# Optimization experiments

Hardware: AMD Instinct MI355X
Metric: run time of the kernel (lower is better)

## Reference

```python
import jax, jax.numpy as jnp
import numpy as np

B, S, D = 4, 2048, 1024
H, K = 16, 64
EPS = 1e-3  # Keras LayerNormalization default epsilon


def setup_inputs() -> dict:
    key = jax.random.key(0)
    ks = jax.random.split(key, 11)
    s = 0.02
    return {
        "x":  jax.random.normal(ks[0], (B, S, D), jnp.float32),
        "Wq": jax.random.normal(ks[1], (D, H, K), jnp.float32) * s,
        "bq": jnp.zeros((H, K), jnp.float32),
        "Wk": jax.random.normal(ks[2], (D, H, K), jnp.float32) * s,
        "bk": jnp.zeros((H, K), jnp.float32),
        "Wv": jax.random.normal(ks[3], (D, H, K), jnp.float32) * s,
        "bv": jnp.zeros((H, K), jnp.float32),
        "Wo": jax.random.normal(ks[4], (H, K, D), jnp.float32) * s,
        "bo": jnp.zeros((D,), jnp.float32),
        "gamma": jnp.ones((D,), jnp.float32),
        "beta":  jnp.zeros((D,), jnp.float32),
    }


def reference(x, Wq, bq, Wk, bk, Wv, bv, Wo, bo, gamma, beta):
    # QKV projections (Keras MHA einsum form): [B,S,D] -> [B,S,H,K]
    q = jnp.einsum("bsd,dhk->bshk", x, Wq) + bq
    k = jnp.einsum("bsd,dhk->bshk", x, Wk) + bk
    v = jnp.einsum("bsd,dhk->bshk", x, Wv) + bv
    scale = 1.0 / jnp.sqrt(jnp.asarray(K, x.dtype))
    scores = jnp.einsum("bqhk,bshk->bhqs", q, k) * scale  # [B,H,S,S]
    attn = jax.nn.softmax(scores, axis=-1)
    ctx = jnp.einsum("bhqs,bshk->bqhk", attn, v)           # [B,S,H,K]
    attn_out = jnp.einsum("bqhk,hkd->bqd", ctx, Wo) + bo   # [B,S,D]
    # residual + LayerNorm (over last axis)
    y = x + attn_out
    mu = jnp.mean(y, axis=-1, keepdims=True)
    var = jnp.mean(jnp.square(y - mu), axis=-1, keepdims=True)
    return (y - mu) * jax.lax.rsqrt(var + EPS) * gamma + beta
```

## Files before the change

### kernel.cpp

```cpp
#include <hip/hip_runtime.h>

typedef float f32x4 __attribute__((ext_vector_type(4)));
typedef float f32x16 __attribute__((ext_vector_type(16)));
typedef __bf16 bf16x8 __attribute__((ext_vector_type(8)));
typedef __bf16 bf16x4 __attribute__((ext_vector_type(4)));
typedef __bf16 bf16x2 __attribute__((ext_vector_type(2)));
typedef unsigned short us4 __attribute__((ext_vector_type(4)));

#define DEV __device__ __forceinline__

DEV unsigned short f2bf(float f) {
  union { float f; unsigned int u; } v; v.f = f;
  unsigned int u = v.u;
  return (unsigned short)((u + 0x7FFFu + ((u >> 16) & 1u)) >> 16);
}

typedef const __attribute__((address_space(1))) void* gvp;
typedef __attribute__((address_space(3))) void* lvp;

DEV void gll16(const void* g, void* l) {
  __builtin_amdgcn_global_load_lds((gvp)g, (lvp)l, 16, 0, 0);
}

DEV float fexp2(float x) { return __builtin_amdgcn_exp2f(x); }

DEV void plswap(unsigned& a, unsigned& b) {
  asm("v_permlane32_swap_b32 %0, %1" : "+v"(a), "+v"(b));
}
DEV float xhalf_sum(float v) {
  union { float f; unsigned u; } a, b;
  a.f = v; b.f = v;
  plswap(a.u, b.u);
  return a.f + b.f;
}

__global__ void k_convert(const float* __restrict__ in, unsigned short* __restrict__ out, int n4) {
  int i = blockIdx.x * blockDim.x + threadIdx.x;
  if (i < n4) {
    float4 v = ((const float4*)in)[i];
    us4 o = { f2bf(v.x), f2bf(v.y), f2bf(v.z), f2bf(v.w) };
    ((us4*)out)[i] = o;
  }
}

__global__ void k_transpose4(const float* __restrict__ w0, const float* __restrict__ w1,
                             const float* __restrict__ w2, const float* __restrict__ w3,
                             unsigned short* __restrict__ o0, unsigned short* __restrict__ o1,
                             unsigned short* __restrict__ o2, unsigned short* __restrict__ o3) {
  const float* in = (blockIdx.z == 0) ? w0 : (blockIdx.z == 1) ? w1 : (blockIdx.z == 2) ? w2 : w3;
  unsigned short* out = (blockIdx.z == 0) ? o0 : (blockIdx.z == 1) ? o1 : (blockIdx.z == 2) ? o2 : o3;
  __shared__ float tile[32][33];
  const int bx = blockIdx.x * 32, by = blockIdx.y * 32;
  const int tx = threadIdx.x, ty = threadIdx.y;
#pragma unroll
  for (int r = 0; r < 4; ++r)
    tile[ty + r * 8][tx] = in[(size_t)(by + ty + r * 8) * 1024 + bx + tx];
  __syncthreads();
#pragma unroll
  for (int r = 0; r < 4; ++r)
    out[(size_t)(bx + ty + r * 8) * 1024 + by + tx] = f2bf(tile[tx][ty + r * 8]);
}

__global__ void k_gemm_qkv(const unsigned short* __restrict__ xb,
                           const unsigned short* __restrict__ wqt,
                           const unsigned short* __restrict__ wkt,
                           const unsigned short* __restrict__ wvt,
                           const float* __restrict__ bq, const float* __restrict__ bk,
                           const float* __restrict__ bv,
                           unsigned short* __restrict__ qb, unsigned short* __restrict__ kb,
                           unsigned short* __restrict__ vtb) {
  __shared__ unsigned short As[128 * 64];
  __shared__ unsigned short Bs[128 * 64];
  const int tid = threadIdx.x;
  const int lane = tid & 63;
  const int wave = tid >> 6;
  const int l15 = lane & 15;
  const int lq  = lane >> 4;
  const int wm = wave >> 1, wn = wave & 1;
  const int z = blockIdx.z;

  const unsigned short* A;
  const unsigned short* Bt;
  int mbase, nbase;
  if (z == 2) { A = wvt; Bt = xb; mbase = blockIdx.y * 128; nbase = blockIdx.x * 128; }
  else        { A = xb; Bt = z ? wkt : wqt; mbase = blockIdx.x * 128; nbase = blockIdx.y * 128; }

  f32x4 acc[4][4] = {};

  for (int kt = 0; kt < 1024; kt += 64) {
    __syncthreads();
#pragma unroll
    for (int c = 0; c < 4; ++c) {
      int e = (c * 256 + tid) * 8;
      int row = e >> 6;
      int o2 = (e * 2) ^ ((row & 7) << 4);
      int col = (o2 >> 1) & 63;
      gll16(A + (size_t)(mbase + row) * 1024 + kt + col,
            As + (c * 256 + (tid & ~63)) * 8);
      gll16(Bt + (size_t)(nbase + row) * 1024 + kt + col,
            Bs + (c * 256 + (tid & ~63)) * 8);
    }
    __syncthreads();
#pragma unroll
    for (int ks = 0; ks < 2; ++ks) {
      bf16x8 af[4], bfv[4];
#pragma unroll
      for (int i = 0; i < 4; ++i) {
        int row = wm * 64 + i * 16 + l15;
        int off = row * 128 + ((((ks << 2) | lq) ^ (row & 7)) << 4);
        af[i] = *(const bf16x8*)((const char*)As + off);
      }
#pragma unroll
      for (int j = 0; j < 4; ++j) {
        int row = wn * 64 + j * 16 + l15;
        int off = row * 128 + ((((ks << 2) | lq) ^ (row & 7)) << 4);
        bfv[j] = *(const bf16x8*)((const char*)Bs + off);
      }
#pragma unroll
      for (int i = 0; i < 4; ++i)
#pragma unroll
        for (int j = 0; j < 4; ++j)
          acc[i][j] = __builtin_amdgcn_mfma_f32_16x16x32_bf16(af[i], bfv[j], acc[i][j], 0, 0, 0);
    }
  }

  const float scale = (z == 0) ? 0.18033688011112042f : 1.0f;
  const float* bias = (z == 0) ? bq : (z == 1) ? bk : bv;
  unsigned short* outp = (z == 0) ? qb : (z == 1) ? kb : vtb;

#pragma unroll
  for (int i = 0; i < 4; ++i) {
#pragma unroll
    for (int j = 0; j < 4; ++j) {
#pragma unroll
      for (int r = 0; r < 4; ++r) {
        int mi = mbase + wm * 64 + i * 16 + lq * 4 + r;
        int nj = nbase + wn * 64 + j * 16 + l15;
        float v = acc[i][j][r];
        if (z < 2) {
          v = (v + bias[nj]) * scale;
          int b = mi >> 11, s = mi & 2047, h = nj >> 6, kk = nj & 63;
          outp[(((size_t)((b << 4) + h) * 2048 + s) << 6) + kk] = f2bf(v);
        } else {
          v = v + bias[mi];
          int h = mi >> 6, d = mi & 63, b = nj >> 11, s = nj & 2047;
          outp[(((size_t)((b << 4) + h) << 6) + d) * 2048 + s] = f2bf(v);
        }
      }
    }
  }
}

__global__ void k_gemm_out(const unsigned short* __restrict__ A,
                           const unsigned short* __restrict__ Bt,
                           const float* __restrict__ bias,
                           float* __restrict__ outp,
                           const float* __restrict__ xres) {
  __shared__ unsigned short As[128 * 64];
  __shared__ unsigned short Bs[128 * 64];
  const int tid = threadIdx.x;
  const int lane = tid & 63;
  const int wave = tid >> 6;
  const int l15 = lane & 15;
  const int lq  = lane >> 4;
  const int wm = wave >> 1, wn = wave & 1;
  const int mbase = blockIdx.x * 128;
  const int nbase = blockIdx.y * 128;

  f32x4 acc[4][4] = {};

  for (int kt = 0; kt < 1024; kt += 64) {
    __syncthreads();
#pragma unroll
    for (int c = 0; c < 4; ++c) {
      int e = (c * 256 + tid) * 8;
      int row = e >> 6;
      int o2 = (e * 2) ^ ((row & 7) << 4);
      int col = (o2 >> 1) & 63;
      gll16(A + (size_t)(mbase + row) * 1024 + kt + col,
            As + (c * 256 + (tid & ~63)) * 8);
      gll16(Bt + (size_t)(nbase + row) * 1024 + kt + col,
            Bs + (c * 256 + (tid & ~63)) * 8);
    }
    __syncthreads();
#pragma unroll
    for (int ks = 0; ks < 2; ++ks) {
      bf16x8 af[4], bfv[4];
#pragma unroll
      for (int i = 0; i < 4; ++i) {
        int row = wm * 64 + i * 16 + l15;
        int off = row * 128 + ((((ks << 2) | lq) ^ (row & 7)) << 4);
        af[i] = *(const bf16x8*)((const char*)As + off);
      }
#pragma unroll
      for (int j = 0; j < 4; ++j) {
        int row = wn * 64 + j * 16 + l15;
        int off = row * 128 + ((((ks << 2) | lq) ^ (row & 7)) << 4);
        bfv[j] = *(const bf16x8*)((const char*)Bs + off);
      }
#pragma unroll
      for (int i = 0; i < 4; ++i)
#pragma unroll
        for (int j = 0; j < 4; ++j)
          acc[i][j] = __builtin_amdgcn_mfma_f32_16x16x32_bf16(af[i], bfv[j], acc[i][j], 0, 0, 0);
    }
  }

#pragma unroll
  for (int i = 0; i < 4; ++i)
#pragma unroll
    for (int j = 0; j < 4; ++j)
#pragma unroll
      for (int r = 0; r < 4; ++r) {
        int mi = mbase + wm * 64 + i * 16 + lq * 4 + r;
        int nj = nbase + wn * 64 + j * 16 + l15;
        size_t idx = (size_t)mi * 1024 + nj;
        outp[idx] = acc[i][j][r] + bias[nj] + xres[idx];
      }
}

__global__ __launch_bounds__(256, 4) void k_attn(const unsigned short* __restrict__ q,
                       const unsigned short* __restrict__ k,
                       const unsigned short* __restrict__ vt,
                       unsigned short* __restrict__ ctx) {
  __shared__ unsigned short KV[2][2][64 * 64];

  const int tid = threadIdx.x;
  const int lane = tid & 63;
  const int wave = tid >> 6;
  const int l31 = lane & 31;
  const int l5 = lane >> 5;

  const int bid = blockIdx.x;
  const int swz = (bid & 7) * 128 + (bid >> 3);
  const int bh = swz >> 4;
  const int qtile = swz & 15;
  const int qbase = qtile * 128;
  const size_t sl = (size_t)bh << 17;

  const int qrow = qbase + wave * 32 + l31;
  bf16x8 qreg[4];
#pragma unroll
  for (int ds = 0; ds < 4; ++ds)
    qreg[ds] = *(const bf16x8*)(q + sl + (size_t)qrow * 64 + ds * 16 + l5 * 8);

#define STAGE_KV(BUF, TT) do {                                                 \
    const int kvb_ = (TT) * 64;                                                \
    _Pragma("unroll")                                                          \
    for (int c = 0; c < 2; ++c) {                                              \
      int e = (c * 256 + tid) * 8;                                             \
      int row_ = e >> 6;                                                       \
      int o2 = (e * 2) ^ ((row_ & 7) << 4);                                    \
      int col_ = (o2 >> 1) & 63;                                               \
      gll16(k + sl + (size_t)(kvb_ + row_) * 64 + col_,                        \
            KV[BUF][0] + (c * 256 + (tid & ~63)) * 8);                         \
      gll16(vt + sl + (size_t)row_ * 2048 + kvb_ + col_,                       \
            KV[BUF][1] + (c * 256 + (tid & ~63)) * 8);                         \
    }                                                                          \
  } while (0)

  STAGE_KV(0, 0);
  __syncthreads();

  f32x16 acc0 = {}, acc1 = {};
  float lrow = 0.f;

  for (int t = 0; t < 32; ++t) {
    const int cur = t & 1;
    if (t < 31) STAGE_KV(cur ^ 1, t + 1);

    const char* Ksc = (const char*)KV[cur][0];
    const char* Vtc = (const char*)KV[cur][1];

    bf16x8 kf0[4], kf1[4];
#pragma unroll
    for (int ds = 0; ds < 4; ++ds) {
      int r0 = l31, r1 = 32 + l31;
      kf0[ds] = *(const bf16x8*)(Ksc + r0 * 128 + ((ds * 32 + l5 * 16) ^ ((r0 & 7) << 4)));
      kf1[ds] = *(const bf16x8*)(Ksc + r1 * 128 + ((ds * 32 + l5 * 16) ^ ((r1 & 7) << 4)));
    }
    f32x16 s0 = {}, s1 = {};
    __builtin_amdgcn_s_setprio(1);
#pragma unroll
    for (int ds = 0; ds < 4; ++ds)
      s0 = __builtin_amdgcn_mfma_f32_32x32x16_bf16(kf0[ds], qreg[ds], s0, 0, 0, 0);
#pragma unroll
    for (int ds = 0; ds < 4; ++ds)
      s1 = __builtin_amdgcn_mfma_f32_32x32x16_bf16(kf1[ds], qreg[ds], s1, 0, 0, 0);
    __builtin_amdgcn_s_setprio(0);
    __builtin_amdgcn_sched_barrier(0);

    unsigned pk0[8], pk1[8];
    float r0s = 0.f, r1s = 0.f, r2s = 0.f, r3s = 0.f;
#pragma unroll
    for (int m = 0; m < 8; ++m) {
      float a0 = fexp2(s0[2 * m]), a1 = fexp2(s0[2 * m + 1]);
      float b0 = fexp2(s1[2 * m]), b1 = fexp2(s1[2 * m + 1]);
      r0s += a0; r1s += a1; r2s += b0; r3s += b1;
      union { bf16x2 v; unsigned u; } ua, ub;
      ua.v = bf16x2{ (__bf16)a0, (__bf16)a1 };
      ub.v = bf16x2{ (__bf16)b0, (__bf16)b1 };
      pk0[m] = ua.u; pk1[m] = ub.u;
    }
    lrow += (r0s + r1s) + (r2s + r3s);
    __builtin_amdgcn_sched_barrier(0);

    bf16x8 av0[4], av1[4];
#pragma unroll
    for (int kvg = 0; kvg < 4; ++kvg) {
      int r0 = l31, r1 = 32 + l31;
      av0[kvg] = *(const bf16x8*)(Vtc + r0 * 128 + ((kvg * 32 + l5 * 16) ^ ((r0 & 7) << 4)));
      av1[kvg] = *(const bf16x8*)(Vtc + r1 * 128 + ((kvg * 32 + l5 * 16) ^ ((r1 & 7) << 4)));
    }
#pragma unroll
    for (int kvh = 0; kvh < 2; ++kvh) {
      unsigned* pk = kvh ? pk1 : pk0;
#pragma unroll
      for (int g = 0; g < 2; ++g) {
        unsigned a0_ = pk[4 * g],     b0_ = pk[4 * g + 2];
        unsigned a1_ = pk[4 * g + 1], b1_ = pk[4 * g + 3];
        plswap(a0_, b0_);
        plswap(a1_, b1_);
        union { unsigned u[4]; bf16x8 v; } pf;
        pf.u[0] = a0_; pf.u[1] = a1_; pf.u[2] = b0_; pf.u[3] = b1_;
        const int kvg = 2 * kvh + g;
        __builtin_amdgcn_s_setprio(1);
        acc0 = __builtin_amdgcn_mfma_f32_32x32x16_bf16(av0[kvg], pf.v, acc0, 0, 0, 0);
        acc1 = __builtin_amdgcn_mfma_f32_32x32x16_bf16(av1[kvg], pf.v, acc1, 0, 0, 0);
        __builtin_amdgcn_s_setprio(0);
      }
    }

    __syncthreads();
  }

  const float inv = 1.f / xhalf_sum(lrow);

  unsigned short* TR = (unsigned short*)KV;
  const int qloc = wave * 32 + l31;
  const int swq = (qloc & 7) << 4;
#pragma unroll
  for (int dh = 0; dh < 2; ++dh) {
    const f32x16& ac = dh ? acc1 : acc0;
#pragma unroll
    for (int g3 = 0; g3 < 4; ++g3) {
      bf16x4 o4 = { (__bf16)(ac[4 * g3] * inv), (__bf16)(ac[4 * g3 + 1] * inv),
                    (__bf16)(ac[4 * g3 + 2] * inv), (__bf16)(ac[4 * g3 + 3] * inv) };
      *(bf16x4*)((char*)TR + qloc * 128 + ((dh * 64 + g3 * 16 + l5 * 8) ^ swq)) = o4;
    }
  }
  __syncthreads();

  const int b = bh >> 4, h = bh & 15;
  {
    int row = tid >> 1, half = tid & 1;
    int sw = (row & 7) << 4;
    unsigned short* gdst = ctx + (size_t)(b * 2048 + qbase + row) * 1024 + h * 64 + half * 32;
#pragma unroll
    for (int i = 0; i < 4; ++i) {
      bf16x8 vv = *(const bf16x8*)((const char*)TR + row * 128 + ((half * 64 + i * 16) ^ sw));
      *(bf16x8*)(gdst + i * 8) = vv;
    }
  }
#undef STAGE_KV
}

__global__ void k_ln(const float* __restrict__ y, const float* __restrict__ gamma,
                     const float* __restrict__ beta, float* __restrict__ out) {
  const int row = blockIdx.x;
  const int tid = threadIdx.x;
  const float4 v = ((const float4*)(y + (size_t)row * 1024))[tid];
  float sum = v.x + v.y + v.z + v.w;
  float sq = v.x * v.x + v.y * v.y + v.z * v.z + v.w * v.w;
#pragma unroll
  for (int m = 1; m <= 32; m <<= 1) {
    sum += __shfl_xor(sum, m);
    sq  += __shfl_xor(sq, m);
  }
  __shared__ float s1[4], s2[4];
  const int wv = tid >> 6, lane = tid & 63;
  if (lane == 0) { s1[wv] = sum; s2[wv] = sq; }
  __syncthreads();
  sum = s1[0] + s1[1] + s1[2] + s1[3];
  sq  = s2[0] + s2[1] + s2[2] + s2[3];
  const float mu = sum * (1.f / 1024.f);
  const float rs = rsqrtf(sq * (1.f / 1024.f) - mu * mu + 1e-3f);
  const float4 g  = ((const float4*)gamma)[tid];
  const float4 bb = ((const float4*)beta)[tid];
  float4 o;
  o.x = (v.x - mu) * rs * g.x + bb.x;
  o.y = (v.y - mu) * rs * g.y + bb.y;
  o.z = (v.z - mu) * rs * g.z + bb.z;
  o.w = (v.w - mu) * rs * g.w + bb.w;
  ((float4*)(out + (size_t)row * 1024))[tid] = o;
}

extern "C" void kernel_launch(void* const* d_in, const int* in_sizes, int n_in,
                              void* d_out, int out_size, void* d_ws, size_t ws_size,
                              hipStream_t stream) {
  const float* x  = (const float*)d_in[0];
  const float* Wq = (const float*)d_in[1];
  const float* bq = (const float*)d_in[2];
  const float* Wk = (const float*)d_in[3];
  const float* bk = (const float*)d_in[4];
  const float* Wv = (const float*)d_in[5];
  const float* bv = (const float*)d_in[6];
  const float* Wo = (const float*)d_in[7];
  const float* bo = (const float*)d_in[8];
  const float* gamma = (const float*)d_in[9];
  const float* beta  = (const float*)d_in[10];
  float* out = (float*)d_out;

  char* ws = (char*)d_ws;
  const size_t MB = 1024 * 1024;
  unsigned short* xb  = (unsigned short*)(ws);
  unsigned short* wqt = (unsigned short*)(ws + 16 * MB);
  unsigned short* wkt = (unsigned short*)(ws + 18 * MB);
  unsigned short* wvt = (unsigned short*)(ws + 20 * MB);
  unsigned short* wot = (unsigned short*)(ws + 22 * MB);
  unsigned short* qb  = (unsigned short*)(ws + 24 * MB);
  unsigned short* kb  = (unsigned short*)(ws + 40 * MB);
  unsigned short* vtb = (unsigned short*)(ws + 56 * MB);
  unsigned short* ctx = (unsigned short*)(ws + 72 * MB);
  float* yb = (float*)(ws + 24 * MB);

  k_convert<<<8192, 256, 0, stream>>>(x, xb, 2097152);
  dim3 tb(32, 8), tg(32, 32, 4);
  k_transpose4<<<tg, tb, 0, stream>>>(Wq, Wk, Wv, Wo, wqt, wkt, wvt, wot);

  k_gemm_qkv<<<dim3(64, 8, 3), 256, 0, stream>>>(xb, wqt, wkt, wvt, bq, bk, bv, qb, kb, vtb);

  k_attn<<<1024, 256, 0, stream>>>(qb, kb, vtb, ctx);

  k_gemm_out<<<dim3(64, 8), 256, 0, stream>>>(ctx, wot, bo, yb, x);

  k_ln<<<8192, 256, 0, stream>>>(yb, gamma, beta, out);
  (void)in_sizes; (void)n_in; (void)out_size; (void)ws_size;
}
```

Measured before the change: 196.6 us.

## Fuse Q and K projections into a double-buffered 256x256 tile GEMM

After: 206.2 us. 4.9% more time.

```diff
diff --git a/kernel.cpp b/kernel.cpp
--- a/kernel.cpp
+++ b/kernel.cpp
@@ -61,14 +61,127 @@
     out[(size_t)(bx + ty + r * 8) * 1024 + by + tx] = f2bf(tile[tx][ty + r * 8]);
 }
 
-__global__ void k_gemm_qkv(const unsigned short* __restrict__ xb,
-                           const unsigned short* __restrict__ wqt,
-                           const unsigned short* __restrict__ wkt,
-                           const unsigned short* __restrict__ wvt,
-                           const float* __restrict__ bq, const float* __restrict__ bk,
-                           const float* __restrict__ bv,
-                           unsigned short* __restrict__ qb, unsigned short* __restrict__ kb,
-                           unsigned short* __restrict__ vtb) {
+__global__ __launch_bounds__(512, 1) void k_gemm8_qk(
+    const unsigned short* __restrict__ A,
+    const unsigned short* __restrict__ Bt,
+    const float* __restrict__ bq, const float* __restrict__ bk,
+    unsigned short* __restrict__ qb, unsigned short* __restrict__ kb) {
+  __shared__ unsigned short LA[2][256 * 64];
+  __shared__ unsigned short LB[2][256 * 64];
+  const int tid = threadIdx.x;
+  const int lane = tid & 63;
+  const int wave = tid >> 6;
+  const int l15 = lane & 15;
+  const int lq = lane >> 4;
+  const int wm = wave >> 2;
+  const int wn = wave & 3;
+
+  const int lin = blockIdx.x + (blockIdx.y << 5);
+  const int swz = (lin & 7) * 32 + (lin >> 3);
+  const int mt = swz & 31, nt = swz >> 5;
+  const int mbase = mt * 256, nbase = nt * 256;
+
+  f32x4 acc[8][4] = {};
+
+#define STAGE8(BUF, TT) do {                                                   \
+    const int kt_ = (TT) * 64;                                                 \
+    _Pragma("unroll")                                                          \
+    for (int c = 0; c < 4; ++c) {                                              \
+      int e = (c * 512 + tid) * 8;                                             \
+      int row_ = e >> 6;                                                       \
+      int o2 = (e * 2) ^ ((row_ & 7) << 4);                                    \
+      int col_ = (o2 >> 1) & 63;                                               \
+      gll16(A + (size_t)(mbase + row_) * 1024 + kt_ + col_,                    \
+            LA[BUF] + (c * 512 + (tid & ~63)) * 8);                            \
+      gll16(Bt + (size_t)(nbase + row_) * 1024 + kt_ + col_,                   \
+            LB[BUF] + (c * 512 + (tid & ~63)) * 8);                            \
+    }                                                                          \
+  } while (0)
+
+#define RDA(MH) do {                                                           \
+    _Pragma("unroll")                                                          \
+    for (int i = 0; i < 4; ++i) {                                              \
+      int lr = wm * 128 + (MH) * 64 + i * 16 + l15;                            \
+      _Pragma("unroll")                                                        \
+      for (int ks = 0; ks < 2; ++ks)                                           \
+        Af[i][ks] = *(const bf16x8*)((const char*)LA[bb] + lr * 128 +          \
+                     ((((ks << 2) | lq) ^ (lr & 7)) << 4));                    \
+    }                                                                          \
+  } while (0)
+
+#define RDB(DST, NH) do {                                                      \
+    _Pragma("unroll")                                                          \
+    for (int j = 0; j < 2; ++j) {                                              \
+      int lr = wn * 64 + (NH) * 32 + j * 16 + l15;                             \
+      _Pragma("unroll")                                                        \
+      for (int ks = 0; ks < 2; ++ks)                                           \
+        DST[j][ks] = *(const bf16x8*)((const char*)LB[bb] + lr * 128 +         \
+                     ((((ks << 2) | lq) ^ (lr & 7)) << 4));                    \
+    }                                                                          \
+  } while (0)
+
+#define MM(MH, NH, BF) do {                                                    \
+    __builtin_amdgcn_s_setprio(1);                                             \
+    _Pragma("unroll")                                                          \
+    for (int i = 0; i < 4; ++i)                                                \
+      _Pragma("unroll")                                                        \
+      for (int j = 0; j < 2; ++j)                                              \
+        _Pragma("unroll")                                                      \
+        for (int ks = 0; ks < 2; ++ks)                                         \
+          acc[(MH) * 4 + i][(NH) * 2 + j] =                                    \
+            __builtin_amdgcn_mfma_f32_16x16x32_bf16(Af[i][ks], BF[j][ks],      \
+                acc[(MH) * 4 + i][(NH) * 2 + j], 0, 0, 0);                     \
+    __builtin_amdgcn_s_setprio(0);                                             \
+  } while (0)
+
+  STAGE8(0, 0);
+  STAGE8(1, 1);
+
+  for (int t = 0; t < 16; ++t) {
+    const int bb = t & 1;
+    if (t == 15) { asm volatile("s_waitcnt vmcnt(0)" ::: "memory"); }
+    else         { asm volatile("s_waitcnt vmcnt(8)" ::: "memory"); }
+    __builtin_amdgcn_s_barrier();
+
+    bf16x8 Af[4][2], B0[2][2], B1[2][2];
+    RDA(0); RDB(B0, 0); MM(0, 0, B0);
+    RDB(B1, 1);         MM(0, 1, B1);
+    RDA(1);             MM(1, 1, B1);
+                        MM(1, 0, B0);
+
+    __builtin_amdgcn_s_barrier();
+    if (t < 14) STAGE8(bb, t + 2);
+  }
+
+  const float scale = 0.18033688011112042f;
+#pragma unroll
+  for (int fi = 0; fi < 8; ++fi) {
+#pragma unroll
+    for (int fj = 0; fj < 4; ++fj) {
+#pragma unroll
+      for (int r = 0; r < 4; ++r) {
+        int mi = mbase + wm * 128 + fi * 16 + lq * 4 + r;
+        int nj = nbase + wn * 64 + fj * 16 + l15;
+        float v = acc[fi][fj][r];
+        int z = nj >> 10, nn = nj & 1023;
+        int h = nn >> 6, kk = nn & 63;
+        int b = mi >> 11, s = mi & 2047;
+        size_t idx = (((size_t)((b << 4) + h) * 2048 + s) << 6) + kk;
+        if (z == 0) qb[idx] = f2bf((v + bq[nn]) * scale);
+        else        kb[idx] = f2bf(v + bk[nn]);
+      }
+    }
+  }
+#undef STAGE8
+#undef RDA
+#undef RDB
+#undef MM
+}
+
+__global__ void k_gemm_vt(const unsigned short* __restrict__ A,
+                          const unsigned short* __restrict__ Bt,
+                          const float* __restrict__ bias,
+                          unsigned short* __restrict__ vtb) {
   __shared__ unsigned short As[128 * 64];
   __shared__ unsigned short Bs[128 * 64];
   const int tid = threadIdx.x;
@@ -77,13 +190,8 @@
   const int l15 = lane & 15;
   const int lq  = lane >> 4;
   const int wm = wave >> 1, wn = wave & 1;
-  const int z = blockIdx.z;
-
-  const unsigned short* A;
-  const unsigned short* Bt;
-  int mbase, nbase;
-  if (z == 2) { A = wvt; Bt = xb; mbase = blockIdx.y * 128; nbase = blockIdx.x * 128; }
-  else        { A = xb; Bt = z ? wkt : wqt; mbase = blockIdx.x * 128; nbase = blockIdx.y * 128; }
+  const int mbase = blockIdx.y * 128;
+  const int nbase = blockIdx.x * 128;
 
   f32x4 acc[4][4] = {};
 
@@ -124,31 +232,18 @@
     }
   }
 
-  const float scale = (z == 0) ? 0.18033688011112042f : 1.0f;
-  const float* bias = (z == 0) ? bq : (z == 1) ? bk : bv;
-  unsigned short* outp = (z == 0) ? qb : (z == 1) ? kb : vtb;
-
-#pragma unroll
-  for (int i = 0; i < 4; ++i) {
-#pragma unroll
-    for (int j = 0; j < 4; ++j) {
+#pragma unroll
+  for (int i = 0; i < 4; ++i)
+#pragma unroll
+    for (int j = 0; j < 4; ++j)
 #pragma unroll
       for (int r = 0; r < 4; ++r) {
         int mi = mbase + wm * 64 + i * 16 + lq * 4 + r;
         int nj = nbase + wn * 64 + j * 16 + l15;
-        float v = acc[i][j][r];
-        if (z < 2) {
-          v = (v + bias[nj]) * scale;
-          int b = mi >> 11, s = mi & 2047, h = nj >> 6, kk = nj & 63;
-          outp[(((size_t)((b << 4) + h) * 2048 + s) << 6) + kk] = f2bf(v);
-        } else {
-          v = v + bias[mi];
-          int h = mi >> 6, d = mi & 63, b = nj >> 11, s = nj & 2047;
-          outp[(((size_t)((b << 4) + h) << 6) + d) * 2048 + s] = f2bf(v);
-        }
-      }
-    }
-  }
+        float v = acc[i][j][r] + bias[mi];
+        int h = mi >> 6, d = mi & 63, b = nj >> 11, s = nj & 2047;
+        vtb[(((size_t)((b << 4) + h) << 6) + d) * 2048 + s] = f2bf(v);
+      }
 }
 
 __global__ void k_gemm_out(const unsigned short* __restrict__ A,
@@ -428,7 +523,8 @@
   dim3 tb(32, 8), tg(32, 32, 4);
   k_transpose4<<<tg, tb, 0, stream>>>(Wq, Wk, Wv, Wo, wqt, wkt, wvt, wot);
 
-  k_gemm_qkv<<<dim3(64, 8, 3), 256, 0, stream>>>(xb, wqt, wkt, wvt, bq, bk, bv, qb, kb, vtb);
+  k_gemm8_qk<<<dim3(32, 8), 512, 0, stream>>>(xb, wqt, bq, bk, qb, kb);
+  k_gemm_vt<<<dim3(64, 8), 256, 0, stream>>>(wvt, xb, bv, vtb);
 
   k_attn<<<1024, 256, 0, stream>>>(qb, kb, vtb, ctx);
 
```

## Stage QKV GEMM epilogue through LDS for vectorized 16-byte global stores

Applied to the files above, without the earlier changes.

Result: faster. 183.3 us (-6.8%).

```diff
diff --git a/kernel.cpp b/kernel.cpp
--- a/kernel.cpp
+++ b/kernel.cpp
@@ -69,8 +69,9 @@
                            const float* __restrict__ bv,
                            unsigned short* __restrict__ qb, unsigned short* __restrict__ kb,
                            unsigned short* __restrict__ vtb) {
-  __shared__ unsigned short As[128 * 64];
-  __shared__ unsigned short Bs[128 * 64];
+  __shared__ unsigned short SM[2][128 * 64];
+  unsigned short* As = SM[0];
+  unsigned short* Bs = SM[1];
   const int tid = threadIdx.x;
   const int lane = tid & 63;
   const int wave = tid >> 6;
@@ -120,7 +121,7 @@
       for (int i = 0; i < 4; ++i)
 #pragma unroll
         for (int j = 0; j < 4; ++j)
-          acc[i][j] = __builtin_amdgcn_mfma_f32_16x16x32_bf16(af[i], bfv[j], acc[i][j], 0, 0, 0);
+          acc[i][j] = __builtin_amdgcn_mfma_f32_16x16x32_bf16(bfv[j], af[i], acc[i][j], 0, 0, 0);
     }
   }
 
@@ -128,26 +129,50 @@
   const float* bias = (z == 0) ? bq : (z == 1) ? bk : bv;
   unsigned short* outp = (z == 0) ? qb : (z == 1) ? kb : vtb;
 
+  float4 bj[4];
+  if (z < 2) {
+#pragma unroll
+    for (int j = 0; j < 4; ++j)
+      bj[j] = *(const float4*)&bias[nbase + wn * 64 + j * 16 + lq * 4];
+  }
+
+  __syncthreads();
+  char* T = (char*)SM;
 #pragma unroll
   for (int i = 0; i < 4; ++i) {
+    const int miL = wm * 64 + i * 16 + l15;
+    const int sw = (miL & 7) << 4;
+    const float bm = (z == 2) ? bias[mbase + miL] : 0.f;
 #pragma unroll
     for (int j = 0; j < 4; ++j) {
+      const int nj2 = (wn * 64 + j * 16 + lq * 4) * 2;
+      bf16x4 p;
 #pragma unroll
       for (int r = 0; r < 4; ++r) {
-        int mi = mbase + wm * 64 + i * 16 + lq * 4 + r;
-        int nj = nbase + wn * 64 + j * 16 + l15;
         float v = acc[i][j][r];
-        if (z < 2) {
-          v = (v + bias[nj]) * scale;
-          int b = mi >> 11, s = mi & 2047, h = nj >> 6, kk = nj & 63;
-          outp[(((size_t)((b << 4) + h) * 2048 + s) << 6) + kk] = f2bf(v);
-        } else {
-          v = v + bias[mi];
-          int h = mi >> 6, d = mi & 63, b = nj >> 11, s = nj & 2047;
-          outp[(((size_t)((b << 4) + h) << 6) + d) * 2048 + s] = f2bf(v);
-        }
-      }
-    }
+        v = (z < 2) ? (v + ((const float*)&bj[j])[r]) * scale : (v + bm);
+        p[r] = (__bf16)v;
+      }
+      *(bf16x4*)(T + miL * 256 + (nj2 ^ sw)) = p;
+    }
+  }
+  __syncthreads();
+
+#pragma unroll
+  for (int c = 0; c < 8; ++c) {
+    const int lin = c * 256 + tid;
+    const int row = lin >> 4;
+    const int s16 = lin & 15;
+    bf16x8 vv = *(const bf16x8*)(T + row * 256 + ((s16 * 16) ^ ((row & 7) << 4)));
+    const int mi = mbase + row;
+    const int nj = nbase + s16 * 8;
+    size_t gaddr;
+    if (z < 2) {
+      gaddr = (((size_t)((mi >> 11) * 16 + (nj >> 6)) * 2048 + (mi & 2047)) << 6) + (nj & 63);
+    } else {
+      gaddr = ((size_t)(((nj >> 11) * 16 + (mi >> 6)) * 64 + (mi & 63))) * 2048 + (nj & 2047);
+    }
+    *(bf16x8*)(outp + gaddr) = vv;
   }
 }
 
```
